# Kernel optimization log

Measured on AMD Instinct MI355X. Metric: run time of the kernel, lower is better.

## Reference

```python
import jax, jax.numpy as jnp
import numpy as np

B_, L_, DM, DI, N, R, K = 2, 1024, 1024, 2048, 16, 64, 4
EPS = 1e-5

def silu(x):
    return x * jax.nn.sigmoid(x)

def causal_conv1d(x, w, b):
    # x: (B,L,D); w: (D,K) depthwise. torch Conv1d(padding=K-1) then slice [:L] == left-pad causal conv.
    L = x.shape[1]
    xp = jnp.pad(x, ((0, 0), (K - 1, 0), (0, 0)))
    y = xp[:, 0:L, :] * w[:, 0]
    for k in range(1, K):
        y = y + xp[:, k:k + L, :] * w[:, k]
    return y + b

def selective_scan(u, delta, A, Bm, Cm, D):
    # u, delta: (B,L,D); A: (D,N); Bm, Cm: (B,L,N)
    dA = jnp.exp(jnp.einsum('bld,dn->bldn', delta, A))
    dBu = jnp.einsum('bld,bln,bld->bldn', delta, Bm, u)
    h0 = jnp.zeros((u.shape[0], u.shape[2], A.shape[1]), u.dtype)
    def step(h, xs):
        dA_t, dBu_t, C_t = xs
        h = dA_t * h + dBu_t
        return h, jnp.einsum('bdn,bn->bd', h, C_t)
    _, ys = jax.lax.scan(step, h0, (jnp.moveaxis(dA, 1, 0), jnp.moveaxis(dBu, 1, 0), jnp.moveaxis(Cm, 1, 0)))
    return jnp.moveaxis(ys, 0, 1) + u * D  # (B,L,D)

def branch(x, conv_w, conv_b, Wx, Wdt, bdt, A_log, D):
    x = silu(causal_conv1d(x, conv_w, conv_b))
    dbl = x @ Wx.T                               # (B,L,R+2N)
    dt, Bm, Cm = dbl[..., :R], dbl[..., R:R + N], dbl[..., R + N:]
    dt = dt @ Wdt.T + bdt                        # dt_proj is Linear WITH bias in source
    delta = jax.nn.softplus(dt + bdt)            # source also passes delta_bias to the scan (bias added twice; faithful)
    A = -jnp.exp(A_log)
    return selective_scan(x, delta, A, Bm, Cm, D)

def reference(a, b, Wi, conv_w, conv_b, Wx, Wdt, bdt, A_log, D,
              conv_w_b, conv_b_b, Wx_b, Wdt_b, bdt_b, A_log_b, D_b, Wo, norm_w):
    xz_a = a @ Wi.T
    x_f, z = xz_a[..., :DI], xz_a[..., DI:]
    y_f = branch(x_f, conv_w, conv_b, Wx, Wdt, bdt, A_log, D)
    xz_b = jnp.flip(b, 1) @ Wi.T
    x_bwd = xz_b[..., :DI]
    y_b = jnp.flip(branch(x_bwd, conv_w_b, conv_b_b, Wx_b, Wdt_b, bdt_b, A_log_b, D_b), 1)
    y = y_f + y_b
    # RMSNormGated, norm_before_gate=False: gate first, then RMSNorm
    g = y * silu(z)
    g = g * jax.lax.rsqrt(jnp.mean(g * g, axis=-1, keepdims=True) + EPS) * norm_w
    return g @ Wo.T

def setup_inputs() -> dict:
    key = jax.random.key(0)
    ks = jax.random.split(key, 16)
    s = 0.02
    def rn(k, shape):
        return jax.random.normal(k, shape, jnp.float32) * s
    def inv_dt(k):
        dt = jnp.exp(jax.random.uniform(k, (DI,)) * (np.log(0.1) - np.log(0.001)) + np.log(0.001))
        dt = jnp.clip(dt, 1e-4, None)
        return dt + jnp.log(-jnp.expm1(-dt))
    A_log = jnp.log(jnp.broadcast_to(jnp.arange(1, N + 1, dtype=jnp.float32), (DI, N)))
    return dict(
        a=jax.random.normal(ks[0], (B_, L_, DM), jnp.float32),
        b=jax.random.normal(ks[1], (B_, L_, DM), jnp.float32),
        Wi=rn(ks[2], (2 * DI, DM)),
        conv_w=rn(ks[3], (DI, K)), conv_b=rn(ks[4], (DI,)),
        Wx=rn(ks[5], (R + 2 * N, DI)), Wdt=rn(ks[6], (DI, R)), bdt=inv_dt(ks[7]),
        A_log=A_log, D=jnp.ones((DI,), jnp.float32),
        conv_w_b=rn(ks[8], (DI, K)), conv_b_b=rn(ks[9], (DI,)),
        Wx_b=rn(ks[10], (R + 2 * N, DI)), Wdt_b=rn(ks[11], (DI, R)), bdt_b=inv_dt(ks[12]),
        A_log_b=A_log, D_b=jnp.ones((DI,), jnp.float32),
        Wo=rn(ks[13], (DM, DI)), norm_w=jnp.ones((DI,), jnp.float32),
    )
```

## Files before the change

kernel.cpp:

```cpp
#include <hip/hip_runtime.h>
#include <hip/hip_bf16.h>
#include <cmath>

#define B_ 2
#define L_ 1024
#define DM 1024
#define DI 2048
#define NS 16
#define RR 64
#define KC 4
#define NCH 64
#define CL (L_ / NCH)
#define NSPLIT 8

using frag8 = __attribute__((ext_vector_type(8))) short;
using facc4 = __attribute__((ext_vector_type(4))) float;
using f32x4 = __attribute__((ext_vector_type(4))) float;

struct alignas(8) S4v { short x, y, z, w; };

__device__ __forceinline__ short f2b(float v) {
    __hip_bfloat16 h = __float2bfloat16(v);
    return *(short*)&h;
}

__device__ __forceinline__ float silu1(float x) {
    return x / (1.f + __expf(-x));
}

__device__ __forceinline__ int swz(int r, int q) {
    return (r * 4 + (q ^ (r & 3))) ^ (((r >> 2) & 1) << 2);
}
__device__ __forceinline__ void swz_src(int l, int& R, int& C) {
    int rho = l >> 2;
    R = rho ^ ((rho >> 2) & 1);
    C = (l & 3) ^ (R & 3);
}

__device__ __forceinline__ void pow4(float qv, f32x4& p0, f32x4& p1, f32x4& p2, f32x4& p3) {
    float q2 = qv * qv, q3 = q2 * qv, q4 = q2 * q2;
    p0 = (f32x4){qv, q2, q3, q4};
    f32x4 s4 = {q4, q4, q4, q4};
    p1 = p0 * s4;
    f32x4 s8 = s4 * s4;
    p2 = p0 * s8;
    p3 = p1 * s8;
}

__device__ __forceinline__ void async_ld16(const void* g, void* l) {
    __builtin_amdgcn_global_load_lds(
        (const __attribute__((address_space(1))) unsigned int*)g,
        (__attribute__((address_space(3))) unsigned int*)l, 16, 0, 0);
}

__device__ __forceinline__ void cvt4(const float* __restrict__ src, size_t si,
                                     short* __restrict__ dst, size_t di2) {
    float4 v = *(const float4*)(src + si);
    S4v r = { f2b(v.x), f2b(v.y), f2b(v.z), f2b(v.w) };
    *(S4v*)(dst + di2) = r;
}

__global__ void cvt_all(const float* __restrict__ a, const float* __restrict__ b,
                        const float* __restrict__ Wi,
                        const float* __restrict__ Wx, const float* __restrict__ Wxb2,
                        const float* __restrict__ Wdt, const float* __restrict__ Wdtb2,
                        const float* __restrict__ Wo,
                        short* __restrict__ abf, short* __restrict__ bbf,
                        short* __restrict__ Wibf,
                        short* __restrict__ Wxbf, short* __restrict__ Wxbbf,
                        short* __restrict__ Wdtbf, short* __restrict__ Wdtbbf,
                        short* __restrict__ Wobf) {
    size_t i = ((size_t)blockIdx.x * 256 + threadIdx.x) * 4;
    const size_t S_ab = (size_t)B_ * L_ * DM;
    if (i < S_ab) { cvt4(a, i, abf, i); return; } i -= S_ab;
    if (i < S_ab) {
        size_t r = i / DM, c = i % DM;
        size_t bb = r / L_, ll = r % L_;
        size_t sr = bb * L_ + (L_ - 1 - ll);
        cvt4(b, sr * DM + c, bbf, i); return;
    } i -= S_ab;
    const size_t S_wi = (size_t)2 * DI * DM;
    if (i < S_wi) { cvt4(Wi, i, Wibf, i); return; } i -= S_wi;
    const size_t S_wx = (size_t)96 * DI;
    if (i < S_wx) { cvt4(Wx, i, Wxbf, i); return; } i -= S_wx;
    if (i < S_wx) { cvt4(Wxb2, i, Wxbbf, i); return; } i -= S_wx;
    const size_t S_wd = (size_t)DI * RR;
    if (i < S_wd) { cvt4(Wdt, i, Wdtbf, i); return; } i -= S_wd;
    if (i < S_wd) { cvt4(Wdtb2, i, Wdtbbf, i); return; } i -= S_wd;
    const size_t S_wo = (size_t)DM * DI;
    if (i < S_wo) cvt4(Wo, i, Wobf, i);
}

template <int BM>
__device__ __forceinline__ void gemm_body(
    const short* A, int lda, const short* W, int ldw, int wRowOff,
    float* C, int ldc, int K, int m0, int n0) {
    constexpr int MF = BM / 32;
    __shared__ __align__(16) short As[2][BM * 32];
    __shared__ __align__(16) short Ws[2][64 * 32];
    const int tid = threadIdx.x;
    const int lane = tid & 63, wv = tid >> 6;
    const int wm = (wv & 1) * (BM / 2), wn = (wv >> 1) * 32;
    const int q = lane >> 4, mr = lane & 15;
    int sR, sC; swz_src(lane, sR, sC);
    const int sg = swz(mr, q) * 8;

    const short* Ag = A + (size_t)(m0 + wv * 16 + sR) * lda + sC * 8;
    const short* Wg = W + (size_t)(n0 + wRowOff + wv * 16 + sR) * ldw + sC * 8;

    facc4 acc[MF][2];
#pragma unroll
    for (int i = 0; i < MF; ++i)
#pragma unroll
        for (int j = 0; j < 2; ++j) acc[i][j] = (facc4){0.f, 0.f, 0.f, 0.f};

    async_ld16(Ag, &As[0][wv * 512]);
    if constexpr (BM == 128) async_ld16(Ag + (size_t)64 * lda, &As[0][wv * 512 + 2048]);
    async_ld16(Wg, &Ws[0][wv * 512]);

    const int nk = K / 32;
    for (int it = 0; it < nk; ++it) {
        const int buf = it & 1;
        __syncthreads();
        if (it + 1 < nk) {
            int k0 = (it + 1) * 32;
            async_ld16(Ag + k0, &As[buf ^ 1][wv * 512]);
            if constexpr (BM == 128)
                async_ld16(Ag + (size_t)64 * lda + k0, &As[buf ^ 1][wv * 512 + 2048]);
            async_ld16(Wg + k0, &Ws[buf ^ 1][wv * 512]);
        }
        frag8 af[MF], wf[2];
#pragma unroll
        for (int t = 0; t < MF; ++t)
            af[t] = *(const frag8*)&As[buf][(wm + t * 16) * 32 + sg];
#pragma unroll
        for (int j = 0; j < 2; ++j)
            wf[j] = *(const frag8*)&Ws[buf][(wn + j * 16) * 32 + sg];
#pragma unroll
        for (int i = 0; i < MF; ++i)
#pragma unroll
            for (int j = 0; j < 2; ++j)
                acc[i][j] = __builtin_amdgcn_mfma_f32_16x16x32_bf16(af[i], wf[j], acc[i][j], 0, 0, 0);
    }
#pragma unroll
    for (int i = 0; i < MF; ++i)
#pragma unroll
        for (int j = 0; j < 2; ++j) {
            int gn = n0 + wn + j * 16 + mr;
#pragma unroll
            for (int e = 0; e < 4; ++e) {
                int gm = m0 + wm + i * 16 + q * 4 + e;
                C[(size_t)gm * ldc + gn] = acc[i][j][e];
            }
        }
}

__global__ __launch_bounds__(256) void gemm_xz_conv(
    const short* __restrict__ abf, const short* __restrict__ bbf,
    const short* __restrict__ Wibf,
    float* __restrict__ UF, float* __restrict__ UB, float* __restrict__ Z,
    short* __restrict__ CFo, short* __restrict__ CBo,
    const float* __restrict__ cwf, const float* __restrict__ cbf2,
    const float* __restrict__ cwb, const float* __restrict__ cbb2) {
    __shared__ __align__(16) char smem[34816];
    short (*As)[4608]  = (short (*)[4608])smem;
    short (*Wsx)[2048] = (short (*)[2048])(smem + 18432);
    short (*Wsz)[2048] = (short (*)[2048])(smem + 26624);
    float (*Xs)[68] = (float (*)[68])smem;

    const int bz = blockIdx.z;
    const bool hasZ = (bz == 0);
    const int tid = threadIdx.x;
    const int lane = tid & 63, wv = tid >> 6;
    const int id = blockIdx.y * gridDim.x + blockIdx.x;
    const int xcd = id & 7, idx = id >> 3;
    const int nt = (xcd & 3) * 8 + (idx & 7);
    const int mt = (xcd >> 2) * 8 + (idx >> 3);
    const int m0 = mt * 128, n0 = nt * 64;
    const bool hasHalo = (m0 % L_ != 0);
    const int wm = (wv & 1) * 64, wn = (wv >> 1) * 32;
    const int q = lane >> 4, mr = lane & 15;
    int sR, sC; swz_src(lane, sR, sC);
    const int sg = swz(mr, q) * 8;

    const short* A = bz ? bbf : abf;

    const short* Ag  = A + (size_t)(m0 + wv * 16 + sR) * DM + sC * 8;
    const short* Agh = A + (size_t)(m0 - 16 + sR) * DM + sC * 8;
    const short* Wgx = Wibf + (size_t)(n0 + wv * 16 + sR) * DM + sC * 8;
    const short* Wgz = Wibf + (size_t)(n0 + DI + wv * 16 + sR) * DM + sC * 8;

    facc4 accx[4][2], accz[4][2], hacc[2];
#pragma unroll
    for (int i = 0; i < 4; ++i)
#pragma unroll
        for (int j = 0; j < 2; ++j) {
            accx[i][j] = (facc4){0.f, 0.f, 0.f, 0.f};
            accz[i][j] = (facc4){0.f, 0.f, 0.f, 0.f};
        }
#pragma unroll
    for (int j = 0; j < 2; ++j) hacc[j] = (facc4){0.f, 0.f, 0.f, 0.f};

    async_ld16(Ag, &As[0][wv * 512]);
    async_ld16(Ag + (size_t)64 * DM, &As[0][wv * 512 + 2048]);
    async_ld16(Wgx, &Wsx[0][wv * 512]);
    if (hasZ) async_ld16(Wgz, &Wsz[0][wv * 512]);
    if (hasHalo && wv == 0) async_ld16(Agh, &As[0][4096]);

    const int nk = DM / 32;
    for (int it = 0; it < nk; ++it) {
        const int buf = it & 1;
        __syncthreads();
        if (it + 1 < nk) {
            int k0 = (it + 1) * 32;
            async_ld16(Ag + k0, &As[buf ^ 1][wv * 512]);
            async_ld16(Ag + (size_t)64 * DM + k0, &As[buf ^ 1][wv * 512 + 2048]);
            async_ld16(Wgx + k0, &Wsx[buf ^ 1][wv * 512]);
            if (hasZ) async_ld16(Wgz + k0, &Wsz[buf ^ 1][wv * 512]);
            if (hasHalo && wv == 0) async_ld16(Agh + k0, &As[buf ^ 1][4096]);
        }
        frag8 af[4], wfx[2], wfz[2];
#pragma unroll
        for (int t = 0; t < 4; ++t)
            af[t] = *(const frag8*)&As[buf][(wm + t * 16) * 32 + sg];
#pragma unroll
        for (int j = 0; j < 2; ++j)
            wfx[j] = *(const frag8*)&Wsx[buf][(wn + j * 16) * 32 + sg];
        if (hasZ) {
#pragma unroll
            for (int j = 0; j < 2; ++j)
                wfz[j] = *(const frag8*)&Wsz[buf][(wn + j * 16) * 32 + sg];
        }
        if (hasHalo && wm == 0) {
            frag8 afh = *(const frag8*)&As[buf][4096 + sg];
#pragma unroll
            for (int j = 0; j < 2; ++j)
                hacc[j] = __builtin_amdgcn_mfma_f32_16x16x32_bf16(afh, wfx[j], hacc[j], 0, 0, 0);
        }
#pragma unroll
        for (int i = 0; i < 4; ++i)
#pragma unroll
            for (int j = 0; j < 2; ++j)
                accx[i][j] = __builtin_amdgcn_mfma_f32_16x16x32_bf16(af[i], wfx[j], accx[i][j], 0, 0, 0);
        if (hasZ) {
#pragma unroll
            for (int i = 0; i < 4; ++i)
#pragma unroll
                for (int j = 0; j < 2; ++j)
                    accz[i][j] = __builtin_amdgcn_mfma_f32_16x16x32_bf16(af[i], wfz[j], accz[i][j], 0, 0, 0);
        }
    }

    if (hasZ) {
#pragma unroll
        for (int i = 0; i < 4; ++i)
#pragma unroll
            for (int j = 0; j < 2; ++j) {
                int gn = n0 + wn + j * 16 + mr;
#pragma unroll
                for (int e = 0; e < 4; ++e) {
                    int gm = m0 + wm + i * 16 + q * 4 + e;
                    Z[(size_t)gm * DI + gn] = accz[i][j][e];
                }
            }
    }

    const float* cw = bz ? cwb : cwf;
    const float* cb = bz ? cbb2 : cbf2;
    float* U   = bz ? UB : UF;
    short* Co  = bz ? CBo : CFo;
    const int col = tid & 63;
    const int dcol = n0 + col;
    const int rg = tid >> 6;
    float4 wd = *(const float4*)(cw + (size_t)dcol * KC);
    float bd = cb[dcol];

    __syncthreads();
#pragma unroll
    for (int p = 0; p < 2; ++p) {
        if (p == 0) {
            if ((wv & 1) == 0) {
#pragma unroll
                for (int j = 0; j < 2; ++j) {
#pragma unroll
                    for (int e = 0; e < 4; ++e)
                        Xs[q * 4 + e][wn + j * 16 + mr] = hacc[j][e];
#pragma unroll
                    for (int i = 0; i < 4; ++i)
#pragma unroll
                        for (int e = 0; e < 4; ++e)
                            Xs[16 + i * 16 + q * 4 + e][wn + j * 16 + mr] = accx[i][j][e];
                }
            }
        } else {
            if ((wv & 1) == 0) {
#pragma unroll
                for (int j = 0; j < 2; ++j)
#pragma unroll
                    for (int e = 0; e < 4; ++e)
                        Xs[q * 4 + e][wn + j * 16 + mr] = accx[3][j][e];
            } else {
#pragma unroll
                for (int j = 0; j < 2; ++j)
#pragma unroll
                    for (int i = 0; i < 4; ++i)
#pragma unroll
                        for (int e = 0; e < 4; ++e)
                            Xs[16 + i * 16 + q * 4 + e][wn + j * 16 + mr] = accx[i][j][e];
            }
        }
        __syncthreads();
#pragma unroll
        for (int rr = 0; rr < 16; ++rr) {
            int rl = rg * 16 + rr;
            float x0 = Xs[13 + rl][col];
            float x1 = Xs[14 + rl][col];
            float x2 = Xs[15 + rl][col];
            float x3 = Xs[16 + rl][col];
            float v = bd + x0 * wd.x + x1 * wd.y + x2 * wd.z + x3 * wd.w;
            float s2 = silu1(v);
            size_t go = (size_t)(m0 + p * 64 + rl) * DI + dcol;
            U[go] = s2;
            Co[go] = f2b(s2);
        }
        if (p == 0) __syncthreads();
    }
}

__global__ __launch_bounds__(256) void gemm_dt(
    const short* __restrict__ dtf, const short* __restrict__ dtb,
    const short* __restrict__ Wf, const short* __restrict__ Wb,
    float* __restrict__ DTF_, float* __restrict__ DTB_) {
    const int bz = blockIdx.z;
    gemm_body<128>(bz ? dtb : dtf, RR, bz ? Wb : Wf, RR, 0,
                   bz ? DTB_ : DTF_, DI, RR, blockIdx.y * 128, blockIdx.x * 64);
}

__global__ __launch_bounds__(256) void gemm_out(
    const short* __restrict__ gbf, const short* __restrict__ Wobf,
    float* __restrict__ out) {
    gemm_body<64>(gbf, DI, Wobf, DI, 0, out, DM, DI, blockIdx.y * 64, blockIdx.x * 64);
}

__global__ __launch_bounds__(256) void gemm_dbl(
    const short* __restrict__ CF, const short* __restrict__ CB,
    const short* __restrict__ Wxf, const short* __restrict__ Wxb,
    float* __restrict__ part) {
    __shared__ __align__(16) short As[2][128 * 32];
    __shared__ __align__(16) short Ws[2][96 * 32];
    const int br = blockIdx.z / NSPLIT, zz = blockIdx.z % NSPLIT;
    const short* A = br ? CB : CF;
    const short* W = br ? Wxb : Wxf;
    constexpr int Kchunk = DI / NSPLIT;
    const int tid = threadIdx.x;
    const int lane = tid & 63, wv = tid >> 6;
    const int m0 = blockIdx.y * 128;
    const int kOff = zz * Kchunk;
    const int wm = (wv & 1) * 64, wn = (wv >> 1) * 48;
    const int q = lane >> 4, mr = lane & 15;
    int sR, sC; swz_src(lane, sR, sC);
    const int sg = swz(mr, q) * 8;

    const short* Ag = A + (size_t)(m0 + wv * 16 + sR) * DI + sC * 8 + kOff;
    const short* Wg = W + (size_t)(wv * 16 + sR) * DI + sC * 8 + kOff;

    facc4 acc[4][3];
#pragma unroll
    for (int i = 0; i < 4; ++i)
#pragma unroll
        for (int j = 0; j < 3; ++j) acc[i][j] = (facc4){0.f, 0.f, 0.f, 0.f};

    async_ld16(Ag, &As[0][wv * 512]);
    async_ld16(Ag + (size_t)64 * DI, &As[0][wv * 512 + 2048]);
    async_ld16(Wg, &Ws[0][wv * 512]);
    if (wv < 2) async_ld16(Wg + (size_t)64 * DI, &Ws[0][wv * 512 + 2048]);

    const int nk = Kchunk / 32;
    for (int it = 0; it < nk; ++it) {
        const int buf = it & 1;
        __syncthreads();
        if (it + 1 < nk) {
            int k0 = (it + 1) * 32;
            async_ld16(Ag + k0, &As[buf ^ 1][wv * 512]);
            async_ld16(Ag + (size_t)64 * DI + k0, &As[buf ^ 1][wv * 512 + 2048]);
            async_ld16(Wg + k0, &Ws[buf ^ 1][wv * 512]);
            if (wv < 2) async_ld16(Wg + (size_t)64 * DI + k0, &Ws[buf ^ 1][wv * 512 + 2048]);
        }
        frag8 af[4], wf[3];
#pragma unroll
        for (int t = 0; t < 4; ++t)
            af[t] = *(const frag8*)&As[buf][(wm + t * 16) * 32 + sg];
#pragma unroll
        for (int j = 0; j < 3; ++j)
            wf[j] = *(const frag8*)&Ws[buf][(wn + j * 16) * 32 + sg];
#pragma unroll
        for (int i = 0; i < 4; ++i)
#pragma unroll
            for (int j = 0; j < 3; ++j)
                acc[i][j] = __builtin_amdgcn_mfma_f32_16x16x32_bf16(af[i], wf[j], acc[i][j], 0, 0, 0);
    }
    float* Cz = part + (size_t)blockIdx.z * (B_ * L_) * 96;
#pragma unroll
    for (int i = 0; i < 4; ++i)
#pragma unroll
        for (int j = 0; j < 3; ++j) {
            int gn = wn + j * 16 + mr;
#pragma unroll
            for (int e = 0; e < 4; ++e) {
                int gm = m0 + wm + i * 16 + q * 4 + e;
                Cz[(size_t)gm * 96 + gn] = acc[i][j][e];
            }
        }
}

__global__ void reduce_dbl(const float* __restrict__ part,
                           float* __restrict__ dblf, float* __restrict__ dblb,
                           short* __restrict__ dtf, short* __restrict__ dtb) {
    int idx = blockIdx.x * blockDim.x + threadIdx.x;
    const int T = B_ * L_ * 96;
    int br = 0;
    if (idx >= T) { br = 1; idx -= T; }
    const float* p = part + (size_t)br * NSPLIT * T;
    float s = 0.f;
#pragma unroll
    for (int z = 0; z < NSPLIT; ++z) s += p[(size_t)z * T + idx];
    (br ? dblb : dblf)[idx] = s;
    int row = idx / 96, col = idx % 96;
    if (col < RR) (br ? dtb : dtf)[(size_t)row * RR + col] = f2b(s);
}

__device__ __forceinline__ float softplus2(float raw, float bd2) {
    float x = raw + bd2;
    return (x > 20.f) ? x : log1pf(__expf(x));
}

__global__ void scan_chunk(float* UF, float* UB, float* DTFm, float* DTBm,
                           const float* bdtf, const float* bdtb,
                           const float* dblF, const float* dblB,
                           const float* Alf, const float* Alb,
                           const float* Dvf, const float* Dvb,
                           float* SF, float* SB) {
    __shared__ __align__(16) float BCs[CL][32];
    const int tid = threadIdx.x;
    const int d = blockIdx.x * 256 + tid;
    const int br = blockIdx.y >> 1, bb = blockIdx.y & 1;
    const int c = blockIdx.z;
    const int l0 = c * CL;
    float* __restrict__ u = br ? UB : UF;
    float* __restrict__ dtm = br ? DTBm : DTFm;
    const float* __restrict__ bdt = br ? bdtb : bdtf;
    const float* __restrict__ dbl = br ? dblB : dblF;
    const float* __restrict__ A_log = br ? Alb : Alf;
    const float* __restrict__ Dv = br ? Dvb : Dvf;
    float* __restrict__ Sbuf = br ? SB : SF;
    {
        int e = tid * 2;
        int row = e >> 5, cc = e & 31;
        *(float2*)&BCs[row][cc] =
            *(const float2*)(dbl + ((size_t)(bb * L_ + l0 + row) * 96 + 64 + cc));
    }
    float Av[NS];
#pragma unroll
    for (int n = 0; n < NS; ++n) Av[n] = -__expf(A_log[d * NS + n]);
    bool structured = true;
#pragma unroll
    for (int n = 1; n < NS; ++n)
        structured = structured &&
            (fabsf(Av[n] - (n + 1) * Av[0]) <= 1e-4f * (n + 1) * fabsf(Av[0]));
    const float bd2 = 2.f * bdt[d];
    const float Dd = Dv[d];
    float cd = 0.f;
    __syncthreads();
    float* __restrict__ up = u + ((size_t)bb * L_ + l0) * DI + d;
    float* __restrict__ dp = dtm + ((size_t)bb * L_ + l0) * DI + d;
    size_t pb = ((size_t)(bb * NCH + c) * NS) * DI + d;

    if (structured) {
        const float Av0 = Av[0];
        f32x4 S4[4];
#pragma unroll
        for (int m = 0; m < 4; ++m) S4[m] = (f32x4){0.f, 0.f, 0.f, 0.f};
        float draw = dp[0], ul = up[0];
        for (int l = 0; l < CL; ++l) {
            float draw_n = 0.f, ul_n = 0.f;
            if (l + 1 < CL) { draw_n = dp[(size_t)(l + 1) * DI]; ul_n = up[(size_t)(l + 1) * DI]; }
            float x = draw + bd2;
            float e = __expf(x);
            float del = (x > 20.f) ? x : __logf(1.f + e);
            cd += del;
            float du = del * ul;
            f32x4 pw0, pw1, pw2, pw3;
            pow4(__expf(del * Av0), pw0, pw1, pw2, pw3);
            const f32x4* BC4 = (const f32x4*)&BCs[l][0];
            f32x4 b0 = BC4[0], b1 = BC4[1], b2 = BC4[2], b3 = BC4[3];
            f32x4 c0 = BC4[4], c1 = BC4[5], c2 = BC4[6], c3 = BC4[7];
            f32x4 du4 = {du, du, du, du};
            S4[0] = pw0 * S4[0] + du4 * b0;
            S4[1] = pw1 * S4[1] + du4 * b1;
            S4[2] = pw2 * S4[2] + du4 * b2;
            S4[3] = pw3 * S4[3] + du4 * b3;
            f32x4 pA = S4[0] * c0 + S4[1] * c1;
            f32x4 pB = S4[2] * c2 + S4[3] * c3;
            f32x4 pv = pA + pB;
            float accv = (pv[0] + pv[1]) + (pv[2] + pv[3]);
            dp[(size_t)l * DI] = cd;
            up[(size_t)l * DI] = accv + ul * Dd;
            draw = draw_n; ul = ul_n;
        }
#pragma unroll
        for (int m = 0; m < 4; ++m)
#pragma unroll
            for (int k2 = 0; k2 < 4; ++k2)
                Sbuf[pb + (size_t)(m * 4 + k2) * DI] = S4[m][k2];
    } else {
        float S[NS];
#pragma unroll
        for (int n = 0; n < NS; ++n) S[n] = 0.f;
        float draw = dp[0], ul = up[0];
        for (int l = 0; l < CL; ++l) {
            float draw_n = 0.f, ul_n = 0.f;
            if (l + 1 < CL) { draw_n = dp[(size_t)(l + 1) * DI]; ul_n = up[(size_t)(l + 1) * DI]; }
            float del = softplus2(draw, bd2);
            cd += del;
            float du = del * ul;
            const float* Brow = &BCs[l][0];
            float pa[4] = {0.f, 0.f, 0.f, 0.f};
#pragma unroll
            for (int j = 0; j < 4; ++j)
#pragma unroll
                for (int k = 0; k < 4; ++k) {
                    int n = j * 4 + k;
                    float dA = __expf(del * Av[n]);
                    S[n] = fmaf(dA, S[n], du * Brow[n]);
                    pa[j] = fmaf(S[n], Brow[16 + n], pa[j]);
                }
            float accv = (pa[0] + pa[1]) + (pa[2] + pa[3]);
            dp[(size_t)l * DI] = cd;
            up[(size_t)l * DI] = accv + ul * Dd;
            draw = draw_n; ul = ul_n;
        }
#pragma unroll
        for (int n = 0; n < NS; ++n)
            Sbuf[pb + (size_t)n * DI] = S[n];
    }
}

__global__ void scan_combine(float* __restrict__ PF, const float* __restrict__ SF,
                             float* __restrict__ PB, const float* __restrict__ SB,
                             const float* __restrict__ DTFm, const float* __restrict__ DTBm,
                             const float* __restrict__ Alf, const float* __restrict__ Alb) {
    int g = blockIdx.x * blockDim.x + threadIdx.x;
    const int T = B_ * NS * DI;
    int br = (g >= T);
    int gg = br ? g - T : g;
    float* __restrict__ P = br ? PB : PF;
    const float* __restrict__ S = br ? SB : SF;
    const float* __restrict__ cdm = br ? DTBm : DTFm;
    const float* __restrict__ Alog = br ? Alb : Alf;
    int d = gg % DI;
    int rest = gg / DI;
    int n = rest % NS, bb = rest / NS;
    const float Avn = -__expf(Alog[d * NS + n]);
    const size_t stride = (size_t)NS * DI;
    const size_t cstride = (size_t)CL * DI;
    size_t o = ((size_t)(bb * NCH) * NS + n) * DI + d;
    const float* cp = cdm + ((size_t)bb * L_ + CL - 1) * DI + d;
    float h = 0.f;
    float Cc[4], Sc[4], Cn[4], Sn[4];
#pragma unroll
    for (int i = 0; i < 4; ++i) {
        Cc[i] = cp[(size_t)i * cstride];
        Sc[i] = S[o + (size_t)i * stride];
    }
    for (int c = 0; c < NCH; c += 4) {
        if (c + 4 < NCH) {
#pragma unroll
            for (int i = 0; i < 4; ++i) {
                Cn[i] = cp[(size_t)(c + i + 4) * cstride];
                Sn[i] = S[o + (size_t)(i + 4) * stride];
            }
        }
#pragma unroll
        for (int i = 0; i < 4; ++i) {
            P[o] = h;
            h = fmaf(__expf(Cc[i] * Avn), h, Sc[i]);
            o += stride;
        }
#pragma unroll
        for (int i = 0; i < 4; ++i) { Cc[i] = Cn[i]; Sc[i] = Sn[i]; }
    }
}

__global__ void scan_apply(float* UF, float* UB,
                           const float* DTFm, const float* DTBm,
                           const float* dblF, const float* dblB,
                           const float* Alf, const float* Alb,
                           const float* PF, const float* PB) {
    __shared__ __align__(16) float Cs[CL][16];
    const int tid = threadIdx.x;
    const int d = blockIdx.x * 256 + tid;
    const int br = blockIdx.y >> 1, bb = blockIdx.y & 1;
    const int c = blockIdx.z + 1;
    const int l0 = c * CL;
    float* __restrict__ y = br ? UB : UF;
    const float* __restrict__ cdm = br ? DTBm : DTFm;
    const float* __restrict__ dbl = br ? dblB : dblF;
    const float* __restrict__ A_log = br ? Alb : Alf;
    const float* __restrict__ Hbuf = br ? PB : PF;
    {
        int row = tid >> 4, cc = tid & 15;
        Cs[row][cc] = dbl[(size_t)(bb * L_ + l0 + row) * 96 + 80 + cc];
    }
    float Av[NS];
#pragma unroll
    for (int n = 0; n < NS; ++n) Av[n] = -__expf(A_log[d * NS + n]);
    bool structured = true;
#pragma unroll
    for (int n = 1; n < NS; ++n)
        structured = structured &&
            (fabsf(Av[n] - (n + 1) * Av[0]) <= 1e-4f * (n + 1) * fabsf(Av[0]));
    size_t pb = ((size_t)(bb * NCH + c) * NS) * DI + d;
    const float* __restrict__ cp = cdm + ((size_t)bb * L_ + l0) * DI + d;
    float* __restrict__ yp = y + ((size_t)bb * L_ + l0) * DI + d;

    if (structured) {
        f32x4 ch4[4];
#pragma unroll
        for (int m = 0; m < 4; ++m)
#pragma unroll
            for (int k2 = 0; k2 < 4; ++k2)
                ch4[m][k2] = Hbuf[pb + (size_t)(m * 4 + k2) * DI];
        __syncthreads();
        const float Av0 = Av[0];
        float cdv = cp[0], yv = yp[0];
        for (int l = 0; l < CL; ++l) {
            float cdn = 0.f, yn = 0.f;
            if (l + 1 < CL) { cdn = cp[(size_t)(l + 1) * DI]; yn = yp[(size_t)(l + 1) * DI]; }
            f32x4 pw0, pw1, pw2, pw3;
            pow4(__expf(cdv * Av0), pw0, pw1, pw2, pw3);
            const f32x4* C4 = (const f32x4*)&Cs[l][0];
            f32x4 pA = pw0 * (C4[0] * ch4[0]) + pw1 * (C4[1] * ch4[1]);
            f32x4 pB = pw2 * (C4[2] * ch4[2]) + pw3 * (C4[3] * ch4[3]);
            f32x4 pv = pA + pB;
            yp[(size_t)l * DI] = yv + (pv[0] + pv[1]) + (pv[2] + pv[3]);
            cdv = cdn; yv = yn;
        }
    } else {
        float chs[NS];
#pragma unroll
        for (int n = 0; n < NS; ++n) chs[n] = Hbuf[pb + (size_t)n * DI];
        __syncthreads();
        float cdv = cp[0], yv = yp[0];
        for (int l = 0; l < CL; ++l) {
            float cdn = 0.f, yn = 0.f;
            if (l + 1 < CL) { cdn = cp[(size_t)(l + 1) * DI]; yn = yp[(size_t)(l + 1) * DI]; }
            const float* Crow = &Cs[l][0];
            float pa[4] = {0.f, 0.f, 0.f, 0.f};
#pragma unroll
            for (int j = 0; j < 4; ++j)
#pragma unroll
                for (int k = 0; k < 4; ++k) {
                    int n = j * 4 + k;
                    pa[j] = fmaf(__expf(cdv * Av[n]), Crow[n] * chs[n], pa[j]);
                }
            yp[(size_t)l * DI] = yv + (pa[0] + pa[1]) + (pa[2] + pa[3]);
            cdv = cdn; yv = yn;
        }
    }
}

__global__ void combine_rms(const float* __restrict__ yf, const float* __restrict__ yb,
                            const float* __restrict__ z,
                            const float* __restrict__ nw,
                            short* __restrict__ g) {
    int row = blockIdx.x;
    int bb = row / L_, l = row % L_;
    int tid = threadIdx.x;
    size_t base = (size_t)row * DI;
    size_t baseb = ((size_t)bb * L_ + (L_ - 1 - l)) * DI;
    float4 gv[2];
    float ss = 0.f;
#pragma unroll
    for (int j = 0; j < 2; ++j) {
        int d = tid * 4 + j * 1024;
        float4 a4 = *(const float4*)(yf + base + d);
        float4 b4 = *(const float4*)(yb + baseb + d);
        float4 z4 = *(const float4*)(z + base + d);
        float4 r;
        r.x = (a4.x + b4.x) * silu1(z4.x);
        r.y = (a4.y + b4.y) * silu1(z4.y);
        r.z = (a4.z + b4.z) * silu1(z4.z);
        r.w = (a4.w + b4.w) * silu1(z4.w);
        gv[j] = r;
        ss += r.x * r.x + r.y * r.y + r.z * r.z + r.w * r.w;
    }
#pragma unroll
    for (int off = 32; off > 0; off >>= 1) ss += __shfl_down(ss, off, 64);
    __shared__ float red[4];
    if ((tid & 63) == 0) red[tid >> 6] = ss;
    __syncthreads();
    float tot = red[0] + red[1] + red[2] + red[3];
    float rms = rsqrtf(tot / (float)DI + 1e-5f);
#pragma unroll
    for (int j = 0; j < 2; ++j) {
        int d = tid * 4 + j * 1024;
        float4 w4 = *(const float4*)(nw + d);
        S4v o = { f2b(gv[j].x * rms * w4.x), f2b(gv[j].y * rms * w4.y),
                  f2b(gv[j].z * rms * w4.z), f2b(gv[j].w * rms * w4.w) };
        *(S4v*)(g + base + d) = o;
    }
}

extern "C" void kernel_launch(void* const* d_in, const int* in_sizes, int n_in,
                              void* d_out, int out_size, void* d_ws, size_t ws_size,
                              hipStream_t stream) {
    const float* a      = (const float*)d_in[0];
    const float* b      = (const float*)d_in[1];
    const float* Wi     = (const float*)d_in[2];
    const float* conv_w = (const float*)d_in[3];
    const float* conv_b = (const float*)d_in[4];
    const float* Wx     = (const float*)d_in[5];
    const float* Wdt    = (const float*)d_in[6];
    const float* bdt    = (const float*)d_in[7];
    const float* A_log  = (const float*)d_in[8];
    const float* Dvec   = (const float*)d_in[9];
    const float* conv_w_b = (const float*)d_in[10];
    const float* conv_b_b = (const float*)d_in[11];
    const float* Wx_b   = (const float*)d_in[12];
    const float* Wdt_b  = (const float*)d_in[13];
    const float* bdt_b  = (const float*)d_in[14];
    const float* A_log_b = (const float*)d_in[15];
    const float* Dvec_b = (const float*)d_in[16];
    const float* Wo     = (const float*)d_in[17];
    const float* nw     = (const float*)d_in[18];
    float* out = (float*)d_out;

    const int M = B_ * L_;
    const size_t BLD = (size_t)M * DI;
    const size_t NDBL = (size_t)M * 96;
    const size_t PSsz = (size_t)NCH * B_ * NS * DI;

    float* f = (float*)d_ws;
    float* Zb   = f;  f += BLD;
    float* UF   = f;  f += BLD;
    float* UB   = f;  f += BLD;
    float* DTF  = f;  f += BLD;
    float* DTB  = f;  f += BLD;
    float* dblf = f;  f += NDBL;
    float* dblb = f;  f += NDBL;
    float* Pf   = f;  f += PSsz;
    float* Sf   = f;  f += PSsz;
    float* Pb   = f;  f += PSsz;
    float* Sb   = f;  f += PSsz;
    float* part = Pf;

    short* s = (short*)f;
    short* abf    = s;  s += (size_t)M * DM;
    short* bbf    = s;  s += (size_t)M * DM;
    short* Wibf   = s;  s += (size_t)2 * DI * DM;
    short* CF     = s;  s += BLD;
    short* CB     = s;  s += BLD;
    short* Wxbf   = s;  s += (size_t)96 * DI;
    short* Wxbbf  = s;  s += (size_t)96 * DI;
    short* Wdtbf  = s;  s += (size_t)DI * RR;
    short* Wdtbbf = s;  s += (size_t)DI * RR;
    short* dtfbf  = s;  s += (size_t)M * RR;
    short* dtbbf  = s;  s += (size_t)M * RR;
    short* Wobf   = s;  s += (size_t)DM * DI;
    short* gbf    = abf;

    dim3 blk(256);

    cvt_all<<<dim3(10880), blk, 0, stream>>>(a, b, Wi, Wx, Wx_b, Wdt, Wdt_b, Wo,
                                             abf, bbf, Wibf, Wxbf, Wxbbf, Wdtbf, Wdtbbf, Wobf);
    gemm_xz_conv<<<dim3(DI / 64, M / 128, 2), blk, 0, stream>>>(
        abf, bbf, Wibf, UF, UB, Zb, CF, CB,
        conv_w, conv_b, conv_w_b, conv_b_b);
    gemm_dbl<<<dim3(1, M / 128, 2 * NSPLIT), blk, 0, stream>>>(CF, CB, Wxbf, Wxbbf, part);
    reduce_dbl<<<dim3(2 * (int)(NDBL / 256)), blk, 0, stream>>>(part, dblf, dblb, dtfbf, dtbbf);
    gemm_dt<<<dim3(DI / 64, M / 128, 2), blk, 0, stream>>>(dtfbf, dtbbf, Wdtbf, Wdtbbf, DTF, DTB);
    scan_chunk<<<dim3(DI / 256, 4, NCH), blk, 0, stream>>>(
        UF, UB, DTF, DTB, bdt, bdt_b, dblf, dblb, A_log, A_log_b, Dvec, Dvec_b,
        Sf, Sb);
    scan_combine<<<dim3(2 * B_ * NS * DI / 256), blk, 0, stream>>>(
        Pf, Sf, Pb, Sb, DTF, DTB, A_log, A_log_b);
    scan_apply<<<dim3(DI / 256, 4, NCH - 1), blk, 0, stream>>>(
        UF, UB, DTF, DTB, dblf, dblb, A_log, A_log_b, Pf, Pb);
    combine_rms<<<dim3(M), blk, 0, stream>>>(UF, UB, Zb, nw, gbf);
    gemm_out<<<dim3(DM / 64, M / 64), blk, 0, stream>>>(gbf, Wobf, out);
}
```

Before: 288.5 us.

## Triple-buffer GEMM shared-memory tiles with explicit vmcnt waits

Moves the bf16 GEMM main loops (the generic gemm_body and the fused xz/conv GEMM) from double to triple buffering, prefetching two k-steps ahead. A partial s_waitcnt vmcnt sized to the per-wave load count replaces the full wait implied by __syncthreads, so loads for later stages stay in flight across the barrier. The aim is to hide global-to-LDS latency better. The cost is more LDS per block (52KB instead of 34KB for the fused kernel), which may reduce occupancy, and the hand-counted vmcnt values must match the loads each wave actually issued.

```diff
diff --git a/kernel.cpp b/kernel.cpp
--- a/kernel.cpp
+++ b/kernel.cpp
@@ -12,6 +12,8 @@
 #define NCH 64
 #define CL (L_ / NCH)
 #define NSPLIT 8
+
+#define VMCNT(N) asm volatile("s_waitcnt vmcnt(" #N ")" ::: "memory")
 
 using frag8 = __attribute__((ext_vector_type(8))) short;
 using facc4 = __attribute__((ext_vector_type(4))) float;
@@ -96,8 +98,8 @@
     const short* A, int lda, const short* W, int ldw, int wRowOff,
     float* C, int ldc, int K, int m0, int n0) {
     constexpr int MF = BM / 32;
-    __shared__ __align__(16) short As[2][BM * 32];
-    __shared__ __align__(16) short Ws[2][64 * 32];
+    __shared__ __align__(16) short As[3][BM * 32];
+    __shared__ __align__(16) short Ws[3][64 * 32];
     const int tid = threadIdx.x;
     const int lane = tid & 63, wv = tid >> 6;
     const int wm = (wv & 1) * (BM / 2), wn = (wv >> 1) * 32;
@@ -114,21 +116,25 @@
 #pragma unroll
         for (int j = 0; j < 2; ++j) acc[i][j] = (facc4){0.f, 0.f, 0.f, 0.f};
 
-    async_ld16(Ag, &As[0][wv * 512]);
-    if constexpr (BM == 128) async_ld16(Ag + (size_t)64 * lda, &As[0][wv * 512 + 2048]);
-    async_ld16(Wg, &Ws[0][wv * 512]);
+    auto stage = [&](int ks, int b) {
+        int k0 = ks * 32;
+        async_ld16(Ag + k0, &As[b][wv * 512]);
+        if constexpr (BM == 128)
+            async_ld16(Ag + (size_t)64 * lda + k0, &As[b][wv * 512 + 2048]);
+        async_ld16(Wg + k0, &Ws[b][wv * 512]);
+    };
 
     const int nk = K / 32;
+    stage(0, 0);
+    if (nk > 1) stage(1, 1);
+    int buf = 0;
     for (int it = 0; it < nk; ++it) {
-        const int buf = it & 1;
-        __syncthreads();
-        if (it + 1 < nk) {
-            int k0 = (it + 1) * 32;
-            async_ld16(Ag + k0, &As[buf ^ 1][wv * 512]);
-            if constexpr (BM == 128)
-                async_ld16(Ag + (size_t)64 * lda + k0, &As[buf ^ 1][wv * 512 + 2048]);
-            async_ld16(Wg + k0, &Ws[buf ^ 1][wv * 512]);
-        }
+        if (it == nk - 1) VMCNT(0);
+        else if (BM == 128) VMCNT(3);
+        else VMCNT(2);
+        __builtin_amdgcn_s_barrier();
+        asm volatile("" ::: "memory");
+        if (it + 2 < nk) { int b2 = buf + 2; if (b2 >= 3) b2 -= 3; stage(it + 2, b2); }
         frag8 af[MF], wf[2];
 #pragma unroll
         for (int t = 0; t < MF; ++t)
@@ -141,6 +147,7 @@
 #pragma unroll
             for (int j = 0; j < 2; ++j)
                 acc[i][j] = __builtin_amdgcn_mfma_f32_16x16x32_bf16(af[i], wf[j], acc[i][j], 0, 0, 0);
+        buf = (buf == 2) ? 0 : buf + 1;
     }
 #pragma unroll
     for (int i = 0; i < MF; ++i)
@@ -162,10 +169,10 @@
     short* __restrict__ CFo, short* __restrict__ CBo,
     const float* __restrict__ cwf, const float* __restrict__ cbf2,
     const float* __restrict__ cwb, const float* __restrict__ cbb2) {
-    __shared__ __align__(16) char smem[34816];
+    __shared__ __align__(16) char smem[52224];
     short (*As)[4608]  = (short (*)[4608])smem;
-    short (*Wsx)[2048] = (short (*)[2048])(smem + 18432);
-    short (*Wsz)[2048] = (short (*)[2048])(smem + 26624);
+    short (*Wsx)[2048] = (short (*)[2048])(smem + 27648);
+    short (*Wsz)[2048] = (short (*)[2048])(smem + 39936);
     float (*Xs)[68] = (float (*)[68])smem;
 
     const int bz = blockIdx.z;
@@ -190,6 +197,8 @@
     const short* Wgx = Wibf + (size_t)(n0 + wv * 16 + sR) * DM + sC * 8;
     const short* Wgz = Wibf + (size_t)(n0 + DI + wv * 16 + sR) * DM + sC * 8;
 
+    const int Kw = (bz ? 3 : 4) + ((hasHalo && wv == 0) ? 1 : 0);
+
     facc4 accx[4][2], accz[4][2], hacc[2];
 #pragma unroll
     for (int i = 0; i < 4; ++i)
@@ -201,24 +210,27 @@
 #pragma unroll
     for (int j = 0; j < 2; ++j) hacc[j] = (facc4){0.f, 0.f, 0.f, 0.f};
 
-    async_ld16(Ag, &As[0][wv * 512]);
-    async_ld16(Ag + (size_t)64 * DM, &As[0][wv * 512 + 2048]);
-    async_ld16(Wgx, &Wsx[0][wv * 512]);
-    if (hasZ) async_ld16(Wgz, &Wsz[0][wv * 512]);
-    if (hasHalo && wv == 0) async_ld16(Agh, &As[0][4096]);
-
+    auto stage = [&](int ks, int b) {
+        int k0 = ks * 32;
+        async_ld16(Ag + k0, &As[b][wv * 512]);
+        async_ld16(Ag + (size_t)64 * DM + k0, &As[b][wv * 512 + 2048]);
+        async_ld16(Wgx + k0, &Wsx[b][wv * 512]);
+        if (hasZ) async_ld16(Wgz + k0, &Wsz[b][wv * 512]);
+        if (hasHalo && wv == 0) async_ld16(Agh + k0, &As[b][4096]);
+    };
+
+    stage(0, 0);
+    stage(1, 1);
     const int nk = DM / 32;
+    int buf = 0;
     for (int it = 0; it < nk; ++it) {
-        const int buf = it & 1;
-        __syncthreads();
-        if (it + 1 < nk) {
-            int k0 = (it + 1) * 32;
-            async_ld16(Ag + k0, &As[buf ^ 1][wv * 512]);
-            async_ld16(Ag + (size_t)64 * DM + k0, &As[buf ^ 1][wv * 512 + 2048]);
-            async_ld16(Wgx + k0, &Wsx[buf ^ 1][wv * 512]);
-            if (hasZ) async_ld16(Wgz + k0, &Wsz[buf ^ 1][wv * 512]);
-            if (hasHalo && wv == 0) async_ld16(Agh + k0, &As[buf ^ 1][4096]);
-        }
+        if (it == nk - 1) VMCNT(0);
+        else if (Kw == 5) VMCNT(5);
+        else if (Kw == 4) VMCNT(4);
+        else VMCNT(3);
+        __builtin_amdgcn_s_barrier();
+        asm volatile("" ::: "memory");
+        if (it + 2 < nk) { int b2 = buf + 2; if (b2 >= 3) b2 -= 3; stage(it + 2, b2); }
         frag8 af[4], wfx[2], wfz[2];
 #pragma unroll
         for (int t = 0; t < 4; ++t)
@@ -249,6 +261,7 @@
                 for (int j = 0; j < 2; ++j)
                     accz[i][j] = __builtin_amdgcn_mfma_f32_16x16x32_bf16(af[i], wfz[j], accz[i][j], 0, 0, 0);
         }
+        buf = (buf == 2) ? 0 : buf + 1;
     }
 
     if (hasZ) {
```

New measurement: 287.1 us. About the same (-0.5%).

## Fuse scan correction into gated RMSNorm and triple-buffer GEMM loads

Applied to the files above, without the earlier changes.

Merges scan_apply and combine_rms into one apply_combine kernel. It adds each row's inter-chunk state correction on the fly and then applies the gate and RMSNorm, so the UF/UB read-modify-write pass and one launch go away. The structured-A check and Av0 are now precomputed once in cvt_all instead of in every block. The GEMM body moves from double to triple buffering with explicit vmcnt waits, keeping two stages in flight. The costs are more LDS per GEMM block, which may lower occupancy, and a fused kernel of only 512 blocks that does per-row barriers and strided P/H reads, which may limit parallelism.

```diff
diff --git a/kernel.cpp b/kernel.cpp
--- a/kernel.cpp
+++ b/kernel.cpp
@@ -13,6 +13,8 @@
 #define CL (L_ / NCH)
 #define NSPLIT 8
 
+#define VMCNT(N) asm volatile("s_waitcnt vmcnt(" #N ")" ::: "memory")
+
 using frag8 = __attribute__((ext_vector_type(8))) short;
 using facc4 = __attribute__((ext_vector_type(4))) float;
 using f32x4 = __attribute__((ext_vector_type(4))) float;
@@ -65,11 +67,13 @@
                         const float* __restrict__ Wx, const float* __restrict__ Wxb2,
                         const float* __restrict__ Wdt, const float* __restrict__ Wdtb2,
                         const float* __restrict__ Wo,
+                        const float* __restrict__ Alf, const float* __restrict__ Alb,
                         short* __restrict__ abf, short* __restrict__ bbf,
                         short* __restrict__ Wibf,
                         short* __restrict__ Wxbf, short* __restrict__ Wxbbf,
                         short* __restrict__ Wdtbf, short* __restrict__ Wdtbbf,
-                        short* __restrict__ Wobf) {
+                        short* __restrict__ Wobf,
+                        float* __restrict__ Av0S, float* __restrict__ stS) {
     size_t i = ((size_t)blockIdx.x * 256 + threadIdx.x) * 4;
     const size_t S_ab = (size_t)B_ * L_ * DM;
     if (i < S_ab) { cvt4(a, i, abf, i); return; } i -= S_ab;
@@ -88,7 +92,24 @@
     if (i < S_wd) { cvt4(Wdt, i, Wdtbf, i); return; } i -= S_wd;
     if (i < S_wd) { cvt4(Wdtb2, i, Wdtbbf, i); return; } i -= S_wd;
     const size_t S_wo = (size_t)DM * DI;
-    if (i < S_wo) cvt4(Wo, i, Wobf, i);
+    if (i < S_wo) { cvt4(Wo, i, Wobf, i); return; } i -= S_wo;
+    const size_t S_av = (size_t)2 * DI;
+    if (i < S_av) {
+#pragma unroll
+        for (int k2 = 0; k2 < 4; ++k2) {
+            size_t idx = i + k2;
+            int br2 = (int)(idx / DI), d2 = (int)(idx % DI);
+            const float* Al = br2 ? Alb : Alf;
+            float Av0 = -__expf(Al[(size_t)d2 * NS]);
+            bool st = true;
+            for (int n = 1; n < NS; ++n) {
+                float Avn = -__expf(Al[(size_t)d2 * NS + n]);
+                st = st && (fabsf(Avn - (n + 1) * Av0) <= 1e-4f * (n + 1) * fabsf(Av0));
+            }
+            Av0S[idx] = Av0;
+            stS[idx] = st ? 1.f : 0.f;
+        }
+    }
 }
 
 template <int BM>
@@ -96,8 +117,8 @@
     const short* A, int lda, const short* W, int ldw, int wRowOff,
     float* C, int ldc, int K, int m0, int n0) {
     constexpr int MF = BM / 32;
-    __shared__ __align__(16) short As[2][BM * 32];
-    __shared__ __align__(16) short Ws[2][64 * 32];
+    __shared__ __align__(16) short As[3][BM * 32];
+    __shared__ __align__(16) short Ws[3][64 * 32];
     const int tid = threadIdx.x;
     const int lane = tid & 63, wv = tid >> 6;
     const int wm = (wv & 1) * (BM / 2), wn = (wv >> 1) * 32;
@@ -114,21 +135,25 @@
 #pragma unroll
         for (int j = 0; j < 2; ++j) acc[i][j] = (facc4){0.f, 0.f, 0.f, 0.f};
 
-    async_ld16(Ag, &As[0][wv * 512]);
-    if constexpr (BM == 128) async_ld16(Ag + (size_t)64 * lda, &As[0][wv * 512 + 2048]);
-    async_ld16(Wg, &Ws[0][wv * 512]);
+    auto stage = [&](int ks, int b) {
+        int k0 = ks * 32;
+        async_ld16(Ag + k0, &As[b][wv * 512]);
+        if constexpr (BM == 128)
+            async_ld16(Ag + (size_t)64 * lda + k0, &As[b][wv * 512 + 2048]);
+        async_ld16(Wg + k0, &Ws[b][wv * 512]);
+    };
 
     const int nk = K / 32;
+    stage(0, 0);
+    if (nk > 1) stage(1, 1);
+    int buf = 0;
     for (int it = 0; it < nk; ++it) {
-        const int buf = it & 1;
-        __syncthreads();
-        if (it + 1 < nk) {
-            int k0 = (it + 1) * 32;
-            async_ld16(Ag + k0, &As[buf ^ 1][wv * 512]);
-            if constexpr (BM == 128)
-                async_ld16(Ag + (size_t)64 * lda + k0, &As[buf ^ 1][wv * 512 + 2048]);
-            async_ld16(Wg + k0, &Ws[buf ^ 1][wv * 512]);
-        }
+        if (it == nk - 1) VMCNT(0);
+        else if (BM == 128) VMCNT(3);
+        else VMCNT(2);
+        __builtin_amdgcn_s_barrier();
+        asm volatile("" ::: "memory");
+        if (it + 2 < nk) { int b2 = buf + 2; if (b2 >= 3) b2 -= 3; stage(it + 2, b2); }
         frag8 af[MF], wf[2];
 #pragma unroll
         for (int t = 0; t < MF; ++t)
@@ -141,6 +166,7 @@
 #pragma unroll
             for (int j = 0; j < 2; ++j)
                 acc[i][j] = __builtin_amdgcn_mfma_f32_16x16x32_bf16(af[i], wf[j], acc[i][j], 0, 0, 0);
+        buf = (buf == 2) ? 0 : buf + 1;
     }
 #pragma unroll
     for (int i = 0; i < MF; ++i)
@@ -591,123 +617,101 @@
     }
 }
 
-__global__ void scan_apply(float* UF, float* UB,
-                           const float* DTFm, const float* DTBm,
-                           const float* dblF, const float* dblB,
-                           const float* Alf, const float* Alb,
-                           const float* PF, const float* PB) {
-    __shared__ __align__(16) float Cs[CL][16];
+__device__ __forceinline__ float corr_term(int d, float cd, float Av0, float st,
+                                           const float* __restrict__ Alog,
+                                           const float* Crow,
+                                           const float* __restrict__ Hcol) {
+    float s0 = 0.f, s1 = 0.f, s2 = 0.f, s3 = 0.f;
+    if (st != 0.f) {
+        f32x4 p0, p1, p2, p3;
+        pow4(__expf(cd * Av0), p0, p1, p2, p3);
+        float pw[16];
+        *(f32x4*)&pw[0] = p0; *(f32x4*)&pw[4] = p1;
+        *(f32x4*)&pw[8] = p2; *(f32x4*)&pw[12] = p3;
+#pragma unroll
+        for (int k = 0; k < 4; ++k) {
+            s0 = fmaf(pw[k],      Crow[k]      * Hcol[(size_t)k * DI],        s0);
+            s1 = fmaf(pw[4 + k],  Crow[4 + k]  * Hcol[(size_t)(4 + k) * DI],  s1);
+            s2 = fmaf(pw[8 + k],  Crow[8 + k]  * Hcol[(size_t)(8 + k) * DI],  s2);
+            s3 = fmaf(pw[12 + k], Crow[12 + k] * Hcol[(size_t)(12 + k) * DI], s3);
+        }
+    } else {
+#pragma unroll
+        for (int k = 0; k < 4; ++k) {
+            s0 = fmaf(__expf(cd * -__expf(Alog[(size_t)d * NS + k])),
+                      Crow[k] * Hcol[(size_t)k * DI], s0);
+            s1 = fmaf(__expf(cd * -__expf(Alog[(size_t)d * NS + 4 + k])),
+                      Crow[4 + k] * Hcol[(size_t)(4 + k) * DI], s1);
+            s2 = fmaf(__expf(cd * -__expf(Alog[(size_t)d * NS + 8 + k])),
+                      Crow[8 + k] * Hcol[(size_t)(8 + k) * DI], s2);
+            s3 = fmaf(__expf(cd * -__expf(Alog[(size_t)d * NS + 12 + k])),
+                      Crow[12 + k] * Hcol[(size_t)(12 + k) * DI], s3);
+        }
+    }
+    return (s0 + s1) + (s2 + s3);
+}
+
+__global__ void apply_combine(
+    const float* __restrict__ UF, const float* __restrict__ UB,
+    const float* __restrict__ Zb,
+    const float* __restrict__ DTF, const float* __restrict__ DTB,
+    const float* __restrict__ dblf, const float* __restrict__ dblb,
+    const float* __restrict__ Pf, const float* __restrict__ Pb,
+    const float* __restrict__ Av0S, const float* __restrict__ stS,
+    const float* __restrict__ Alf, const float* __restrict__ Alb,
+    const float* __restrict__ nw,
+    short* __restrict__ g) {
+    const int c = blockIdx.x;
+    const int rp = blockIdx.y;
+    const int bb = blockIdx.z;
+    const int cb = NCH - 1 - c;
     const int tid = threadIdx.x;
-    const int d = blockIdx.x * 256 + tid;
-    const int br = blockIdx.y >> 1, bb = blockIdx.y & 1;
-    const int c = blockIdx.z + 1;
-    const int l0 = c * CL;
-    float* __restrict__ y = br ? UB : UF;
-    const float* __restrict__ cdm = br ? DTBm : DTFm;
-    const float* __restrict__ dbl = br ? dblB : dblF;
-    const float* __restrict__ A_log = br ? Alb : Alf;
-    const float* __restrict__ Hbuf = br ? PB : PF;
-    {
-        int row = tid >> 4, cc = tid & 15;
-        Cs[row][cc] = dbl[(size_t)(bb * L_ + l0 + row) * 96 + 80 + cc];
-    }
-    float Av[NS];
-#pragma unroll
-    for (int n = 0; n < NS; ++n) Av[n] = -__expf(A_log[d * NS + n]);
-    bool structured = true;
-#pragma unroll
-    for (int n = 1; n < NS; ++n)
-        structured = structured &&
-            (fabsf(Av[n] - (n + 1) * Av[0]) <= 1e-4f * (n + 1) * fabsf(Av[0]));
-    size_t pb = ((size_t)(bb * NCH + c) * NS) * DI + d;
-    const float* __restrict__ cp = cdm + ((size_t)bb * L_ + l0) * DI + d;
-    float* __restrict__ yp = y + ((size_t)bb * L_ + l0) * DI + d;
-
-    if (structured) {
-        f32x4 ch4[4];
-#pragma unroll
-        for (int m = 0; m < 4; ++m)
-#pragma unroll
-            for (int k2 = 0; k2 < 4; ++k2)
-                ch4[m][k2] = Hbuf[pb + (size_t)(m * 4 + k2) * DI];
+    __shared__ float CsF[4][16], CsB[4][16], red[4];
+    if (tid < 64) {
+        int rr = tid >> 4, n = tid & 15;
+        int lf = c * CL + rp * 4 + rr;
+        CsF[rr][n] = dblf[(size_t)(bb * L_ + lf) * 96 + 80 + n];
+    } else if (tid < 128) {
+        int t2 = tid - 64;
+        int rr = t2 >> 4, n = t2 & 15;
+        int lf = c * CL + rp * 4 + rr;
+        CsB[rr][n] = dblb[(size_t)(bb * L_ + (L_ - 1 - lf)) * 96 + 80 + n];
+    }
+    __syncthreads();
+    const size_t hfb = ((size_t)(bb * NCH + c) * NS) * DI;
+    const size_t hbb = ((size_t)(bb * NCH + cb) * NS) * DI;
+    for (int rr = 0; rr < 4; ++rr) {
+        int lf = c * CL + rp * 4 + rr;
+        size_t rf = (size_t)bb * L_ + lf;
+        size_t rb = (size_t)bb * L_ + (L_ - 1 - lf);
+        float gv[8];
+        float ss = 0.f;
+#pragma unroll
+        for (int k = 0; k < 8; ++k) {
+            int d = tid + k * 256;
+            float cf = corr_term(d, DTF[rf * DI + d], Av0S[d], stS[d], Alf,
+                                 &CsF[rr][0], Pf + hfb + d);
+            float cbv = corr_term(d, DTB[rb * DI + d], Av0S[DI + d], stS[DI + d], Alb,
+                                  &CsB[rr][0], Pb + hbb + d);
+            float yf = UF[rf * DI + d] + cf;
+            float yb = UB[rb * DI + d] + cbv;
+            float zz = Zb[rf * DI + d];
+            float gg = (yf + yb) * silu1(zz);
+            gv[k] = gg;
+            ss += gg * gg;
+        }
+#pragma unroll
+        for (int off = 32; off > 0; off >>= 1) ss += __shfl_down(ss, off, 64);
+        if ((tid & 63) == 0) red[tid >> 6] = ss;
         __syncthreads();
-        const float Av0 = Av[0];
-        float cdv = cp[0], yv = yp[0];
-        for (int l = 0; l < CL; ++l) {
-            float cdn = 0.f, yn = 0.f;
-            if (l + 1 < CL) { cdn = cp[(size_t)(l + 1) * DI]; yn = yp[(size_t)(l + 1) * DI]; }
-            f32x4 pw0, pw1, pw2, pw3;
-            pow4(__expf(cdv * Av0), pw0, pw1, pw2, pw3);
-            const f32x4* C4 = (const f32x4*)&Cs[l][0];
-            f32x4 pA = pw0 * (C4[0] * ch4[0]) + pw1 * (C4[1] * ch4[1]);
-            f32x4 pB = pw2 * (C4[2] * ch4[2]) + pw3 * (C4[3] * ch4[3]);
-            f32x4 pv = pA + pB;
-            yp[(size_t)l * DI] = yv + (pv[0] + pv[1]) + (pv[2] + pv[3]);
-            cdv = cdn; yv = yn;
-        }
-    } else {
-        float chs[NS];
-#pragma unroll
-        for (int n = 0; n < NS; ++n) chs[n] = Hbuf[pb + (size_t)n * DI];
+        float tot = red[0] + red[1] + red[2] + red[3];
+        float rms = rsqrtf(tot / (float)DI + 1e-5f);
+#pragma unroll
+        for (int k = 0; k < 8; ++k) {
+            int d = tid + k * 256;
+            g[rf * DI + d] = f2b(gv[k] * rms * nw[d]);
+        }
         __syncthreads();
-        float cdv = cp[0], yv = yp[0];
-        for (int l = 0; l < CL; ++l) {
-            float cdn = 0.f, yn = 0.f;
-            if (l + 1 < CL) { cdn = cp[(size_t)(l + 1) * DI]; yn = yp[(size_t)(l + 1) * DI]; }
-            const float* Crow = &Cs[l][0];
-            float pa[4] = {0.f, 0.f, 0.f, 0.f};
-#pragma unroll
-            for (int j = 0; j < 4; ++j)
-#pragma unroll
-                for (int k = 0; k < 4; ++k) {
-                    int n = j * 4 + k;
-                    pa[j] = fmaf(__expf(cdv * Av[n]), Crow[n] * chs[n], pa[j]);
-                }
-            yp[(size_t)l * DI] = yv + (pa[0] + pa[1]) + (pa[2] + pa[3]);
-            cdv = cdn; yv = yn;
-        }
-    }
-}
-
-__global__ void combine_rms(const float* __restrict__ yf, const float* __restrict__ yb,
-                            const float* __restrict__ z,
-                            const float* __restrict__ nw,
-                            short* __restrict__ g) {
-    int row = blockIdx.x;
-    int bb = row / L_, l = row % L_;
-    int tid = threadIdx.x;
-    size_t base = (size_t)row * DI;
-    size_t baseb = ((size_t)bb * L_ + (L_ - 1 - l)) * DI;
-    float4 gv[2];
-    float ss = 0.f;
-#pragma unroll
-    for (int j = 0; j < 2; ++j) {
-        int d = tid * 4 + j * 1024;
-        float4 a4 = *(const float4*)(yf + base + d);
-        float4 b4 = *(const float4*)(yb + baseb + d);
-        float4 z4 = *(const float4*)(z + base + d);
-        float4 r;
-        r.x = (a4.x + b4.x) * silu1(z4.x);
-        r.y = (a4.y + b4.y) * silu1(z4.y);
-        r.z = (a4.z + b4.z) * silu1(z4.z);
-        r.w = (a4.w + b4.w) * silu1(z4.w);
-        gv[j] = r;
-        ss += r.x * r.x + r.y * r.y + r.z * r.z + r.w * r.w;
-    }
-#pragma unroll
-    for (int off = 32; off > 0; off >>= 1) ss += __shfl_down(ss, off, 64);
-    __shared__ float red[4];
-    if ((tid & 63) == 0) red[tid >> 6] = ss;
-    __syncthreads();
-    float tot = red[0] + red[1] + red[2] + red[3];
-    float rms = rsqrtf(tot / (float)DI + 1e-5f);
-#pragma unroll
-    for (int j = 0; j < 2; ++j) {
-        int d = tid * 4 + j * 1024;
-        float4 w4 = *(const float4*)(nw + d);
-        S4v o = { f2b(gv[j].x * rms * w4.x), f2b(gv[j].y * rms * w4.y),
-                  f2b(gv[j].z * rms * w4.z), f2b(gv[j].w * rms * w4.w) };
-        *(S4v*)(g + base + d) = o;
     }
 }
 
@@ -752,6 +756,8 @@
     float* Sf   = f;  f += PSsz;
     float* Pb   = f;  f += PSsz;
     float* Sb   = f;  f += PSsz;
+    float* Av0S = f;  f += (size_t)2 * DI;
+    float* stS  = f;  f += (size_t)2 * DI;
     float* part = Pf;
 
     short* s = (short*)f;
@@ -771,8 +777,10 @@
 
     dim3 blk(256);
 
-    cvt_all<<<dim3(10880), blk, 0, stream>>>(a, b, Wi, Wx, Wx_b, Wdt, Wdt_b, Wo,
-                                             abf, bbf, Wibf, Wxbf, Wxbbf, Wdtbf, Wdtbbf, Wobf);
+    cvt_all<<<dim3(10884), blk, 0, stream>>>(a, b, Wi, Wx, Wx_b, Wdt, Wdt_b, Wo,
+                                             A_log, A_log_b,
+                                             abf, bbf, Wibf, Wxbf, Wxbbf, Wdtbf, Wdtbbf,
+                                             Wobf, Av0S, stS);
     gemm_xz_conv<<<dim3(DI / 64, M / 128, 2), blk, 0, stream>>>(
         abf, bbf, Wibf, UF, UB, Zb, CF, CB,
         conv_w, conv_b, conv_w_b, conv_b_b);
@@ -784,8 +792,8 @@
         Sf, Sb);
     scan_combine<<<dim3(2 * B_ * NS * DI / 256), blk, 0, stream>>>(
         Pf, Sf, Pb, Sb, DTF, DTB, A_log, A_log_b);
-    scan_apply<<<dim3(DI / 256, 4, NCH - 1), blk, 0, stream>>>(
-        UF, UB, DTF, DTB, dblf, dblb, A_log, A_log_b, Pf, Pb);
-    combine_rms<<<dim3(M), blk, 0, stream>>>(UF, UB, Zb, nw, gbf);
+    apply_combine<<<dim3(NCH, 4, B_), blk, 0, stream>>>(
+        UF, UB, Zb, DTF, DTB, dblf, dblb, Pf, Pb, Av0S, stS,
+        A_log, A_log_b, nw, gbf);
     gemm_out<<<dim3(DM / 64, M / 64), blk, 0, stream>>>(gbf, Wobf, out);
 }
```

After: 1.004 ms. 248% more time.
